# Optimization experiments

Hardware: AMD Instinct MI355X
Metric: run time of the kernel (lower is better)

Reference implementation:

```python
import jax, jax.numpy as jnp
import numpy as np

# physics constants (match init_kwargs)
DT = 1.0 / 60.0
G_ACC = 9.81
RHO = 1.225
CD = 0.47
NU = 0.001
B, N, GRID = 512, 64, 16


def _norm(x):
    return jnp.linalg.norm(x, axis=-1, keepdims=True)


def _deriv(pos, vel, rot, omega, mass, inertia, contacts, fluid_v,
           Fext, tau, log_A, log_k, log_b, conv_w):
    g_vec = jnp.array([0.0, 0.0, -G_ACC], dtype=pos.dtype)
    Fg = mass[..., None] * g_vec                                  # [B,N,3]
    A = jax.nn.softplus(log_A).reshape(1, -1, 1)
    vm = jnp.maximum(_norm(vel), 1e-6)
    Fd = -0.5 * RHO * CD * A * vm * vel                           # drag
    k = jax.nn.softplus(log_k)
    b = jax.nn.softplus(log_b)
    d_ij = pos[:, None, :, :] - pos[:, :, None, :]                # [B,N,N,3] = p_j - p_i
    dist = jnp.maximum(_norm(d_ij), 1e-6)
    n_hat = d_ij / dist
    pen = jax.nn.relu(1.0 - dist[..., 0])                         # penetration depth
    dvel = vel[:, None, :, :] - vel[:, :, None, :]                # v_j - v_i
    Fc = (k * pen[..., None] * n_hat + b * dvel * contacts[..., None]).sum(axis=2)
    dv = (Fext + Fg + Fd + Fc) / mass[..., None]
    Io = inertia * omega
    domega = (tau - jnp.cross(omega, Io)) / jnp.maximum(inertia, 1e-6)
    w, x, y, z = rot[..., 0], rot[..., 1], rot[..., 2], rot[..., 3]
    ox, oy, oz = omega[..., 0], omega[..., 1], omega[..., 2]
    drot = 0.5 * jnp.stack([
        -x * ox - y * oy - z * oz,
        w * ox + y * oz - z * oy,
        w * oy - x * oz + z * ox,
        w * oz + x * oy - y * ox], axis=-1)
    P_in = (Fext * vel).sum((-1, -2))
    P_dis = -(Fd * vel).sum((-1, -2))
    dE = P_in - P_dis
    Bsz = fluid_v.shape[0]
    u = fluid_v.reshape(Bsz, GRID, GRID, GRID, 3).transpose(0, 4, 1, 2, 3)  # NCDHW
    dfluid = NU * jax.lax.conv_general_dilated(
        u, conv_w, window_strides=(1, 1, 1), padding=[(1, 1)] * 3,
        feature_group_count=3,
        dimension_numbers=('NCDHW', 'OIDHW', 'NCDHW'))
    dfluid = dfluid.transpose(0, 2, 3, 4, 1).reshape(Bsz, GRID ** 3, 3)
    return vel, dv, drot, domega, dE, dfluid


def _quat_normalize(q):
    return q / jnp.maximum(_norm(q), 1e-12)


def _apply(pos, vel, rot, omega, fluid_v, dt, dp, dv, dr, dw, dfluid):
    npos = pos + dt * dp
    nvel = vel + dt * dv
    nrot = _quat_normalize(rot + dt * dr)
    nomega = omega + dt * dw
    new_u = fluid_v + dt * dfluid
    nfluid = new_u - new_u.mean(axis=1, keepdims=True)
    return npos, nvel, nrot, nomega, nfluid


def _forward(pos, vel, rot, omega, mass, inertia, contacts, energy, fluid_v,
             Fext, tau, log_A, log_k, log_b, conv_w):
    dt = DT
    params = (mass, inertia, contacts)

    def deriv(p, v, r, o, fv):
        return _deriv(p, v, r, o, mass, inertia, contacts, fv,
                      Fext, tau, log_A, log_k, log_b, conv_w)

    k1 = deriv(pos, vel, rot, omega, fluid_v)
    s2 = _apply(pos, vel, rot, omega, fluid_v, dt / 2, k1[0], k1[1], k1[2], k1[3], k1[5])
    k2 = deriv(*s2)
    s3 = _apply(pos, vel, rot, omega, fluid_v, dt / 2, k2[0], k2[1], k2[2], k2[3], k2[5])
    k3 = deriv(*s3)
    s4 = _apply(pos, vel, rot, omega, fluid_v, dt, k3[0], k3[1], k3[2], k3[3], k3[5])
    k4 = deriv(*s4)

    def rk4c(y, a, b_, c, d):
        return y + dt / 6 * (a + 2 * b_ + 2 * c + d)

    npos = rk4c(pos, k1[0], k2[0], k3[0], k4[0])
    nvel = rk4c(vel, k1[1], k2[1], k3[1], k4[1])
    nrot = _quat_normalize(rk4c(rot, k1[2], k2[2], k3[2], k4[2]))
    nomega = rk4c(omega, k1[3], k2[3], k3[3], k4[3])
    nenergy = rk4c(energy, k1[4], k2[4], k3[4], k4[4])
    nforces = Fext + mass[..., None] * k1[1]
    raw_fluid = rk4c(fluid_v, k1[5], k2[5], k3[5], k4[5])
    nfluid = raw_fluid - raw_fluid.mean(axis=1, keepdims=True)
    Bsz = pos.shape[0]
    # flatten new state: [pos, vel, rot, omega, forces, energy, fluid_v]
    return jnp.concatenate([
        npos.reshape(Bsz, -1), nvel.reshape(Bsz, -1), nrot.reshape(Bsz, -1),
        nomega.reshape(Bsz, -1), nforces.reshape(Bsz, -1),
        nenergy[:, None], nfluid.reshape(Bsz, -1)], axis=-1)


def setup_inputs() -> dict:
    key = jax.random.key(0)
    ks = jax.random.split(key, 12)
    rot = jax.random.normal(ks[2], (B, N, 4), dtype=jnp.float32)
    rot = rot / jnp.maximum(jnp.linalg.norm(rot, axis=-1, keepdims=True), 1e-12)
    return {
        'pos': 2.0 * jax.random.normal(ks[0], (B, N, 3), dtype=jnp.float32),
        'vel': jax.random.normal(ks[1], (B, N, 3), dtype=jnp.float32),
        'rot': rot,
        'omega': jax.random.normal(ks[3], (B, N, 3), dtype=jnp.float32),
        'mass': 0.5 + jax.random.uniform(ks[4], (B, N), dtype=jnp.float32),
        'inertia': 0.05 + 0.1 * jax.random.uniform(ks[5], (B, N, 3), dtype=jnp.float32),
        'contacts': jax.random.uniform(ks[6], (B, N, N), dtype=jnp.float32),
        'energy': jnp.zeros((B,), dtype=jnp.float32),
        'fluid_v': jax.random.normal(ks[7], (B, GRID ** 3, 3), dtype=jnp.float32),
        'Fext': jax.random.normal(ks[8], (B, N, 3), dtype=jnp.float32),
        'tau': jax.random.normal(ks[9], (B, N, 3), dtype=jnp.float32),
        'log_A': jnp.zeros((N,), dtype=jnp.float32),
        'log_k': jnp.full((1,), np.log(1000.0), dtype=jnp.float32),
        'log_b': jnp.full((1,), np.log(10.0), dtype=jnp.float32),
        'conv_w': 0.1 * jax.random.normal(ks[10], (3, 1, 3, 3, 3), dtype=jnp.float32),
    }


def reference(pos, vel, rot, omega, mass, inertia, contacts, energy, fluid_v,
              Fext, tau, log_A, log_k, log_b, conv_w):
    return _forward(pos, vel, rot, omega, mass, inertia, contacts, energy,
                    fluid_v, Fext, tau, log_A, log_k, log_b, conv_w)
```

## Files before the change

kernel.cpp:

```cpp
#include <hip/hip_runtime.h>

#define DT (1.0f/60.0f)
#define G_ACC 9.81f
#define RHO 1.225f
#define CD_ 0.47f
#define NU 0.001f

__device__ __forceinline__ float softplus_f(float x) {
    return log1pf(expf(-fabsf(x))) + fmaxf(x, 0.0f);
}

#define RL(v, l) __int_as_float(__builtin_amdgcn_readlane(__float_as_int(v), (l)))

__device__ __forceinline__ float dpp_xm(float v) {
    return __int_as_float(__builtin_amdgcn_update_dpp(0, __float_as_int(v), 0x111, 0xf, 0xf, true));
}
__device__ __forceinline__ float dpp_xp(float v) {
    return __int_as_float(__builtin_amdgcn_update_dpp(0, __float_as_int(v), 0x101, 0xf, 0xf, true));
}

__global__ __launch_bounds__(256) void fused_kernel(
    const float* __restrict__ pos, const float* __restrict__ vel,
    const float* __restrict__ rot, const float* __restrict__ omega,
    const float* __restrict__ mass, const float* __restrict__ inertia,
    const float* __restrict__ contacts, const float* __restrict__ energy,
    const float* __restrict__ fluid, const float* __restrict__ Fext,
    const float* __restrict__ tau, const float* __restrict__ log_A,
    const float* __restrict__ log_k, const float* __restrict__ log_b,
    const float* __restrict__ conv_w, float* __restrict__ out)
{
    __shared__ float smem[4384];
    const int t = threadIdx.x;

    if (blockIdx.x < 1536) {
        const int b  = blockIdx.x & 511;
        const int ch = blockIdx.x >> 9;
        const int x  = t & 15, y = t >> 4, wv = t >> 6;
        float* u   = smem;
        float* wch = smem + 4352;
        float* red = smem + 4380;
        if (t < 27) wch[t] = conv_w[ch*27 + t];

        const int lb = t*17;
        const float* fb = fluid + (size_t)b*12288 + 3*t + ch;
        float base[16], acc[16];
        #pragma unroll
        for (int z = 0; z < 16; ++z) {
            float v = fb[z*768];
            base[z] = v; acc[z] = 0.f; u[lb + z] = v;
        }
        __syncthreads();

        const float mm = (y > 0)  ? 1.f : 0.f;
        const float pm = (y < 15) ? 1.f : 0.f;
        const float xm = (x > 0)  ? 1.f : 0.f;
        const float xp = (x < 15) ? 1.f : 0.f;
        const int   cm = (y > 0)  ? lb - 272 : lb;
        const int   cp = (y < 15) ? lb + 272 : lb;

        float Sdz[3];
        #pragma unroll
        for (int dz = 0; dz < 3; ++dz) {
            float a0 = wch[dz*9+0]*xm + wch[dz*9+1] + wch[dz*9+2]*xp;
            float a1 = wch[dz*9+3]*xm + wch[dz*9+4] + wch[dz*9+5]*xp;
            float a2 = wch[dz*9+6]*xm + wch[dz*9+7] + wch[dz*9+8]*xp;
            Sdz[dz] = mm*a0 + a1 + pm*a2;
        }
        const float SzLo  = Sdz[1] + Sdz[2];
        const float SzMid = Sdz[0] + Sdz[1] + Sdz[2];
        const float SzHi  = Sdz[0] + Sdz[1];
        const float* W = wch + 0;

        const float wgt[4] = {1.f, 2.f, 2.f, 1.f};
        const float hs[3]  = {DT*0.5f, DT*0.5f, DT};
        float mean = 0.f;

        #define ACC3(c, wi) { \
            float w0_ = W[wi], w1_ = W[9+(wi)], w2_ = W[18+(wi)]; \
            _Pragma("unroll") for (int z = 0; z < 16; ++z) o[z] += w1_ * (c)[z]; \
            _Pragma("unroll") for (int z = 1; z < 16; ++z) o[z] += w0_ * (c)[z-1]; \
            _Pragma("unroll") for (int z = 0; z < 15; ++z) o[z] += w2_ * (c)[z+1]; }

        for (int s = 0; s < 4; ++s) {
            float o[16];
            #pragma unroll
            for (int z = 0; z < 16; ++z) o[z] = 0.f;

            {
                float c0[16], cl[16], cr[16];
                #pragma unroll
                for (int z = 0; z < 16; ++z) c0[z] = u[lb + z];
                #pragma unroll
                for (int z = 0; z < 16; ++z) { cl[z] = dpp_xm(c0[z]); cr[z] = dpp_xp(c0[z]); }
                ACC3(c0, 4); ACC3(cl, 3); ACC3(cr, 5);
            }
            {
                float c0[16], cl[16], cr[16];
                #pragma unroll
                for (int z = 0; z < 16; ++z) c0[z] = u[cm + z] * mm;
                #pragma unroll
                for (int z = 0; z < 16; ++z) { cl[z] = dpp_xm(c0[z]); cr[z] = dpp_xp(c0[z]); }
                ACC3(c0, 1); ACC3(cl, 0); ACC3(cr, 2);
            }
            {
                float c0[16], cl[16], cr[16];
                #pragma unroll
                for (int z = 0; z < 16; ++z) c0[z] = u[cp + z] * pm;
                #pragma unroll
                for (int z = 0; z < 16; ++z) { cl[z] = dpp_xm(c0[z]); cr[z] = dpp_xp(c0[z]); }
                ACC3(c0, 7); ACC3(cl, 6); ACC3(cr, 8);
            }

            float w = wgt[s];
            if (s < 3) {
                float h = hs[s], ps = 0.f, wn[16];
                #pragma unroll
                for (int z = 0; z < 16; ++z) {
                    float Sz = (z == 0) ? SzLo : ((z == 15) ? SzHi : SzMid);
                    float k = NU * (o[z] - mean * Sz);
                    acc[z] += w * k;
                    wn[z] = base[z] + h * k;
                    ps += wn[z];
                }
                #pragma unroll
                for (int off = 32; off > 0; off >>= 1) ps += __shfl_xor(ps, off, 64);
                __syncthreads();
                #pragma unroll
                for (int z = 0; z < 16; ++z) u[lb + z] = wn[z];
                if ((t & 63) == 0) red[wv] = ps;
                __syncthreads();
                mean = (red[0] + red[1] + red[2] + red[3]) * (1.0f/4096.0f);
            } else {
                #pragma unroll
                for (int z = 0; z < 16; ++z) {
                    float Sz = (z == 0) ? SzLo : ((z == 15) ? SzHi : SzMid);
                    acc[z] += w * NU * (o[z] - mean * Sz);
                }
            }
        }
        #undef ACC3

        float raw[16], ps = 0.f;
        #pragma unroll
        for (int z = 0; z < 16; ++z) { raw[z] = base[z] + (DT/6.0f)*acc[z]; ps += raw[z]; }
        #pragma unroll
        for (int off = 32; off > 0; off >>= 1) ps += __shfl_xor(ps, off, 64);
        __syncthreads();
        if ((t & 63) == 0) red[wv] = ps;
        __syncthreads();
        float mn = (red[0] + red[1] + red[2] + red[3]) * (1.0f/4096.0f);

        float* ob = out + (size_t)b*13313 + 1025 + 3*t + ch;
        #pragma unroll
        for (int z = 0; z < 16; ++z) ob[z*768] = raw[z] - mn;
        return;
    }

    const int b = blockIdx.x - 1536;
    const int q = t >> 6;
    const int i = t & 63;
    #define SF(buf, qq, idx) smem[(buf)*768 + (qq)*192 + (idx)]

    const float* cbase = contacts + (size_t)b*4096 + (size_t)i*64 + q*16;
    float4 cA = ((const float4*)cbase)[0];
    float4 cB = ((const float4*)cbase)[1];
    float4 cC = ((const float4*)cbase)[2];
    float4 cD = ((const float4*)cbase)[3];
    float cj[16] = {cA.x,cA.y,cA.z,cA.w, cB.x,cB.y,cB.z,cB.w,
                    cC.x,cC.y,cC.z,cC.w, cD.x,cD.y,cD.z,cD.w};

    const size_t p3 = ((size_t)b*64 + i)*3;
    const size_t p4 = ((size_t)b*64 + i)*4;
    float bpx=pos[p3],   bpy=pos[p3+1],   bpz=pos[p3+2];
    float bvx=vel[p3],   bvy=vel[p3+1],   bvz=vel[p3+2];
    float brw=rot[p4],   brx=rot[p4+1],   bry=rot[p4+2],  brz=rot[p4+3];
    float box=omega[p3], boy=omega[p3+1], boz=omega[p3+2];
    float m  = mass[(size_t)b*64+i];
    float Ix=inertia[p3], Iy=inertia[p3+1], Iz=inertia[p3+2];
    float Fex=Fext[p3],   Fey=Fext[p3+1],   Fez=Fext[p3+2];
    float tx=tau[p3],     ty=tau[p3+1],     tz=tau[p3+2];
    float Ai = softplus_f(log_A[i]);
    float kc = softplus_f(log_k[0]);
    float bc = softplus_f(log_b[0]);
    float dragc = -0.5f * RHO * CD_ * Ai;
    float invm  = 1.0f / m;
    float iIx = 1.0f/fmaxf(Ix,1e-6f), iIy = 1.0f/fmaxf(Iy,1e-6f), iIz = 1.0f/fmaxf(Iz,1e-6f);

    float cpx=bpx, cpy=bpy, cpz=bpz;
    float cvx=bvx, cvy=bvy, cvz=bvz;
    float crw=brw, crx=brx, cry=bry, crz=brz;
    float cox=box, coy=boy, coz=boz;

    float apx=0,apy=0,apz=0, avx=0,avy=0,avz=0;
    float arw=0,arx=0,ary=0,arz=0, awx=0,awy=0,awz=0;
    float eacc=0.f;
    float k1vx=0,k1vy=0,k1vz=0;

    const float wgt[4] = {1.f, 2.f, 2.f, 1.f};
    const float hs[4]  = {DT*0.5f, DT*0.5f, DT, 0.f};
    const int j0 = q << 4;

    for (int s = 0; s < 4; ++s) {
        float Fcx=0.f, Fcy=0.f, Fcz=0.f;
        #pragma unroll
        for (int jj = 0; jj < 16; ++jj) {
            const int j = j0 + jj;
            float pjx = RL(cpx, j), pjy = RL(cpy, j), pjz = RL(cpz, j);
            float vjx = RL(cvx, j), vjy = RL(cvy, j), vjz = RL(cvz, j);
            float dx = pjx - cpx, dy = pjy - cpy, dz = pjz - cpz;
            float d2 = dx*dx + dy*dy + dz*dz;
            float dist = fmaxf(sqrtf(d2), 1e-6f);
            float pen  = fmaxf(1.0f - dist, 0.0f);
            float coef = kc * pen * __builtin_amdgcn_rcpf(dist);
            float cbj  = bc * cj[jj];
            Fcx += coef*dx + cbj*(vjx - cvx);
            Fcy += coef*dy + cbj*(vjy - cvy);
            Fcz += coef*dz + cbj*(vjz - cvz);
        }
        const int buf = s & 1;
        SF(buf, q, i*3+0) = Fcx;
        SF(buf, q, i*3+1) = Fcy;
        SF(buf, q, i*3+2) = Fcz;
        __syncthreads();
        Fcx = SF(buf,0,i*3+0) + SF(buf,1,i*3+0) + SF(buf,2,i*3+0) + SF(buf,3,i*3+0);
        Fcy = SF(buf,0,i*3+1) + SF(buf,1,i*3+1) + SF(buf,2,i*3+1) + SF(buf,3,i*3+1);
        Fcz = SF(buf,0,i*3+2) + SF(buf,1,i*3+2) + SF(buf,2,i*3+2) + SF(buf,3,i*3+2);

        float vm = fmaxf(sqrtf(cvx*cvx+cvy*cvy+cvz*cvz), 1e-6f);
        float dc = dragc * vm;
        float Fdx = dc*cvx, Fdy = dc*cvy, Fdz = dc*cvz;

        float dvx = (Fex + Fdx + Fcx) * invm;
        float dvy = (Fey + Fdy + Fcy) * invm;
        float dvz = (Fez - m*G_ACC + Fdz + Fcz) * invm;

        float dqw = 0.5f*(-crx*cox - cry*coy - crz*coz);
        float dqx = 0.5f*( crw*cox + cry*coz - crz*coy);
        float dqy = 0.5f*( crw*coy - crx*coz + crz*cox);
        float dqz = 0.5f*( crw*coz + crx*coy - cry*cox);

        float Iox = Ix*cox, Ioy = Iy*coy, Ioz = Iz*coz;
        float cxv = coy*Ioz - coz*Ioy;
        float cyv = coz*Iox - cox*Ioz;
        float czv = cox*Ioy - coy*Iox;
        float dwx = (tx - cxv) * iIx;
        float dwy = (ty - cyv) * iIy;
        float dwz = (tz - czv) * iIz;

        float ei = (Fex+Fdx)*cvx + (Fey+Fdy)*cvy + (Fez+Fdz)*cvz;
        #pragma unroll
        for (int off = 32; off > 0; off >>= 1) ei += __shfl_xor(ei, off, 64);

        float w = wgt[s];
        eacc += w * ei;
        if (s == 0) { k1vx=dvx; k1vy=dvy; k1vz=dvz; }
        apx += w*cvx; apy += w*cvy; apz += w*cvz;
        avx += w*dvx; avy += w*dvy; avz += w*dvz;
        arw += w*dqw; arx += w*dqx; ary += w*dqy; arz += w*dqz;
        awx += w*dwx; awy += w*dwy; awz += w*dwz;

        if (s < 3) {
            float h = hs[s];
            float npx = bpx + h*cvx, npy = bpy + h*cvy, npz = bpz + h*cvz;
            cvx = bvx + h*dvx; cvy = bvy + h*dvy; cvz = bvz + h*dvz;
            cpx = npx; cpy = npy; cpz = npz;
            float qw = brw + h*dqw, qx = brx + h*dqx, qy = bry + h*dqy, qz = brz + h*dqz;
            float iqn = 1.0f / fmaxf(sqrtf(qw*qw+qx*qx+qy*qy+qz*qz), 1e-12f);
            crw = qw*iqn; crx = qx*iqn; cry = qy*iqn; crz = qz*iqn;
            cox = box + h*dwx; coy = boy + h*dwy; coz = boz + h*dwz;
        }
    }

    if (q == 0) {
        const float s6 = DT / 6.0f;
        float* ob = out + (size_t)b * 13313;
        ob[      i*3+0] = bpx + s6*apx;  ob[      i*3+1] = bpy + s6*apy;  ob[      i*3+2] = bpz + s6*apz;
        ob[192 + i*3+0] = bvx + s6*avx;  ob[192 + i*3+1] = bvy + s6*avy;  ob[192 + i*3+2] = bvz + s6*avz;
        {
            float qw=brw+s6*arw, qx=brx+s6*arx, qy=bry+s6*ary, qz=brz+s6*arz;
            float iq = 1.0f / fmaxf(sqrtf(qw*qw+qx*qx+qy*qy+qz*qz), 1e-12f);
            ob[384 + i*4+0]=qw*iq; ob[384 + i*4+1]=qx*iq; ob[384 + i*4+2]=qy*iq; ob[384 + i*4+3]=qz*iq;
        }
        ob[640 + i*3+0] = box + s6*awx;  ob[640 + i*3+1] = boy + s6*awy;  ob[640 + i*3+2] = boz + s6*awz;
        ob[832 + i*3+0] = Fex + m*k1vx;  ob[832 + i*3+1] = Fey + m*k1vy;  ob[832 + i*3+2] = Fez + m*k1vz;
        if (i == 0) ob[1024] = energy[b] + s6*eacc;
    }
    #undef SF
}

extern "C" void kernel_launch(void* const* d_in, const int* in_sizes, int n_in,
                              void* d_out, int out_size, void* d_ws, size_t ws_size,
                              hipStream_t stream) {
    const float* pos      = (const float*)d_in[0];
    const float* vel      = (const float*)d_in[1];
    const float* rot      = (const float*)d_in[2];
    const float* omega    = (const float*)d_in[3];
    const float* mass     = (const float*)d_in[4];
    const float* inertia  = (const float*)d_in[5];
    const float* contacts = (const float*)d_in[6];
    const float* energy   = (const float*)d_in[7];
    const float* fluid_v  = (const float*)d_in[8];
    const float* Fext     = (const float*)d_in[9];
    const float* tau      = (const float*)d_in[10];
    const float* log_A    = (const float*)d_in[11];
    const float* log_k    = (const float*)d_in[12];
    const float* log_b    = (const float*)d_in[13];
    const float* conv_w   = (const float*)d_in[14];
    float* out = (float*)d_out;

    fused_kernel<<<dim3(2048), dim3(256), 0, stream>>>(
        pos, vel, rot, omega, mass, inertia, contacts, energy, fluid_v,
        Fext, tau, log_A, log_k, log_b, conv_w, out);
}
```

Baseline: 159.0 us.

## Process all three fluid channels in one block per batch

Each fluid block now loops over the three velocity channels sequentially instead of launching one block per channel, cutting the grid from 2048 to 1024 blocks. Output stores are interleaved across channels, so each thread writes three contiguous floats per z rather than strided single floats. The cost is less parallelism, longer serial work per block, and more live registers (raw0, raw1, rloc), which may lower occupancy.

```diff
diff --git a/kernel.cpp b/kernel.cpp
--- a/kernel.cpp
+++ b/kernel.cpp
@@ -32,24 +32,13 @@
     __shared__ float smem[4384];
     const int t = threadIdx.x;
 
-    if (blockIdx.x < 1536) {
-        const int b  = blockIdx.x & 511;
-        const int ch = blockIdx.x >> 9;
+    if (blockIdx.x < 512) {
+        const int b  = blockIdx.x;
         const int x  = t & 15, y = t >> 4, wv = t >> 6;
         float* u   = smem;
         float* wch = smem + 4352;
         float* red = smem + 4380;
-        if (t < 27) wch[t] = conv_w[ch*27 + t];
-
         const int lb = t*17;
-        const float* fb = fluid + (size_t)b*12288 + 3*t + ch;
-        float base[16], acc[16];
-        #pragma unroll
-        for (int z = 0; z < 16; ++z) {
-            float v = fb[z*768];
-            base[z] = v; acc[z] = 0.f; u[lb + z] = v;
-        }
-        __syncthreads();
 
         const float mm = (y > 0)  ? 1.f : 0.f;
         const float pm = (y < 15) ? 1.f : 0.f;
@@ -58,22 +47,11 @@
         const int   cm = (y > 0)  ? lb - 272 : lb;
         const int   cp = (y < 15) ? lb + 272 : lb;
 
-        float Sdz[3];
-        #pragma unroll
-        for (int dz = 0; dz < 3; ++dz) {
-            float a0 = wch[dz*9+0]*xm + wch[dz*9+1] + wch[dz*9+2]*xp;
-            float a1 = wch[dz*9+3]*xm + wch[dz*9+4] + wch[dz*9+5]*xp;
-            float a2 = wch[dz*9+6]*xm + wch[dz*9+7] + wch[dz*9+8]*xp;
-            Sdz[dz] = mm*a0 + a1 + pm*a2;
-        }
-        const float SzLo  = Sdz[1] + Sdz[2];
-        const float SzMid = Sdz[0] + Sdz[1] + Sdz[2];
-        const float SzHi  = Sdz[0] + Sdz[1];
-        const float* W = wch + 0;
-
         const float wgt[4] = {1.f, 2.f, 2.f, 1.f};
         const float hs[3]  = {DT*0.5f, DT*0.5f, DT};
-        float mean = 0.f;
+
+        float raw0[16], raw1[16], rloc[16];
+        float mn0 = 0.f, mn1 = 0.f, mn2 = 0.f;
 
         #define ACC3(c, wi) { \
             float w0_ = W[wi], w1_ = W[9+(wi)], w2_ = W[18+(wi)]; \
@@ -81,82 +59,124 @@
             _Pragma("unroll") for (int z = 1; z < 16; ++z) o[z] += w0_ * (c)[z-1]; \
             _Pragma("unroll") for (int z = 0; z < 15; ++z) o[z] += w2_ * (c)[z+1]; }
 
-        for (int s = 0; s < 4; ++s) {
-            float o[16];
+        for (int ch = 0; ch < 3; ++ch) {
+            if (t < 27) wch[t] = conv_w[ch*27 + t];
+            const float* fb = fluid + (size_t)b*12288 + 3*t + ch;
+            float base[16], acc[16];
             #pragma unroll
-            for (int z = 0; z < 16; ++z) o[z] = 0.f;
-
-            {
-                float c0[16], cl[16], cr[16];
+            for (int z = 0; z < 16; ++z) {
+                float v = fb[z*768];
+                base[z] = v; acc[z] = 0.f; u[lb + z] = v;
+            }
+            __syncthreads();
+
+            float Sdz[3];
+            #pragma unroll
+            for (int dz = 0; dz < 3; ++dz) {
+                float a0 = wch[dz*9+0]*xm + wch[dz*9+1] + wch[dz*9+2]*xp;
+                float a1 = wch[dz*9+3]*xm + wch[dz*9+4] + wch[dz*9+5]*xp;
+                float a2 = wch[dz*9+6]*xm + wch[dz*9+7] + wch[dz*9+8]*xp;
+                Sdz[dz] = mm*a0 + a1 + pm*a2;
+            }
+            const float SzLo  = Sdz[1] + Sdz[2];
+            const float SzMid = Sdz[0] + Sdz[1] + Sdz[2];
+            const float SzHi  = Sdz[0] + Sdz[1];
+            const float* W = wch;
+            float mean = 0.f;
+
+            for (int s = 0; s < 4; ++s) {
+                float o[16];
                 #pragma unroll
-                for (int z = 0; z < 16; ++z) c0[z] = u[lb + z];
-                #pragma unroll
-                for (int z = 0; z < 16; ++z) { cl[z] = dpp_xm(c0[z]); cr[z] = dpp_xp(c0[z]); }
-                ACC3(c0, 4); ACC3(cl, 3); ACC3(cr, 5);
-            }
-            {
-                float c0[16], cl[16], cr[16];
-                #pragma unroll
-                for (int z = 0; z < 16; ++z) c0[z] = u[cm + z] * mm;
-                #pragma unroll
-                for (int z = 0; z < 16; ++z) { cl[z] = dpp_xm(c0[z]); cr[z] = dpp_xp(c0[z]); }
-                ACC3(c0, 1); ACC3(cl, 0); ACC3(cr, 2);
-            }
-            {
-                float c0[16], cl[16], cr[16];
-                #pragma unroll
-                for (int z = 0; z < 16; ++z) c0[z] = u[cp + z] * pm;
-                #pragma unroll
-                for (int z = 0; z < 16; ++z) { cl[z] = dpp_xm(c0[z]); cr[z] = dpp_xp(c0[z]); }
-                ACC3(c0, 7); ACC3(cl, 6); ACC3(cr, 8);
-            }
-
-            float w = wgt[s];
-            if (s < 3) {
-                float h = hs[s], ps = 0.f, wn[16];
-                #pragma unroll
-                for (int z = 0; z < 16; ++z) {
-                    float Sz = (z == 0) ? SzLo : ((z == 15) ? SzHi : SzMid);
-                    float k = NU * (o[z] - mean * Sz);
-                    acc[z] += w * k;
-                    wn[z] = base[z] + h * k;
-                    ps += wn[z];
+                for (int z = 0; z < 16; ++z) o[z] = 0.f;
+
+                {
+                    float c0[16], cl[16], cr[16];
+                    #pragma unroll
+                    for (int z = 0; z < 16; ++z) c0[z] = u[lb + z];
+                    #pragma unroll
+                    for (int z = 0; z < 16; ++z) { cl[z] = dpp_xm(c0[z]); cr[z] = dpp_xp(c0[z]); }
+                    ACC3(c0, 4); ACC3(cl, 3); ACC3(cr, 5);
                 }
-                #pragma unroll
-                for (int off = 32; off > 0; off >>= 1) ps += __shfl_xor(ps, off, 64);
-                __syncthreads();
-                #pragma unroll
-                for (int z = 0; z < 16; ++z) u[lb + z] = wn[z];
-                if ((t & 63) == 0) red[wv] = ps;
-                __syncthreads();
-                mean = (red[0] + red[1] + red[2] + red[3]) * (1.0f/4096.0f);
-            } else {
-                #pragma unroll
-                for (int z = 0; z < 16; ++z) {
-                    float Sz = (z == 0) ? SzLo : ((z == 15) ? SzHi : SzMid);
-                    acc[z] += w * NU * (o[z] - mean * Sz);
+                {
+                    float c0[16], cl[16], cr[16];
+                    #pragma unroll
+                    for (int z = 0; z < 16; ++z) c0[z] = u[cm + z] * mm;
+                    #pragma unroll
+                    for (int z = 0; z < 16; ++z) { cl[z] = dpp_xm(c0[z]); cr[z] = dpp_xp(c0[z]); }
+                    ACC3(c0, 1); ACC3(cl, 0); ACC3(cr, 2);
+                }
+                {
+                    float c0[16], cl[16], cr[16];
+                    #pragma unroll
+                    for (int z = 0; z < 16; ++z) c0[z] = u[cp + z] * pm;
+                    #pragma unroll
+                    for (int z = 0; z < 16; ++z) { cl[z] = dpp_xm(c0[z]); cr[z] = dpp_xp(c0[z]); }
+                    ACC3(c0, 7); ACC3(cl, 6); ACC3(cr, 8);
+                }
+
+                float w = wgt[s];
+                if (s < 3) {
+                    float h = hs[s], ps = 0.f, wn[16];
+                    #pragma unroll
+                    for (int z = 0; z < 16; ++z) {
+                        float Sz = (z == 0) ? SzLo : ((z == 15) ? SzHi : SzMid);
+                        float k = NU * (o[z] - mean * Sz);
+                        acc[z] += w * k;
+                        wn[z] = base[z] + h * k;
+                        ps += wn[z];
+                    }
+                    #pragma unroll
+                    for (int off = 32; off > 0; off >>= 1) ps += __shfl_xor(ps, off, 64);
+                    __syncthreads();
+                    #pragma unroll
+                    for (int z = 0; z < 16; ++z) u[lb + z] = wn[z];
+                    if ((t & 63) == 0) red[wv] = ps;
+                    __syncthreads();
+                    mean = (red[0] + red[1] + red[2] + red[3]) * (1.0f/4096.0f);
+                } else {
+                    #pragma unroll
+                    for (int z = 0; z < 16; ++z) {
+                        float Sz = (z == 0) ? SzLo : ((z == 15) ? SzHi : SzMid);
+                        acc[z] += w * NU * (o[z] - mean * Sz);
+                    }
                 }
             }
+
+            float ps = 0.f;
+            #pragma unroll
+            for (int z = 0; z < 16; ++z) { rloc[z] = base[z] + (DT/6.0f)*acc[z]; ps += rloc[z]; }
+            #pragma unroll
+            for (int off = 32; off > 0; off >>= 1) ps += __shfl_xor(ps, off, 64);
+            __syncthreads();
+            if ((t & 63) == 0) red[wv] = ps;
+            __syncthreads();
+            float mn = (red[0] + red[1] + red[2] + red[3]) * (1.0f/4096.0f);
+
+            if (ch == 0) {
+                #pragma unroll
+                for (int z = 0; z < 16; ++z) raw0[z] = rloc[z];
+                mn0 = mn;
+            } else if (ch == 1) {
+                #pragma unroll
+                for (int z = 0; z < 16; ++z) raw1[z] = rloc[z];
+                mn1 = mn;
+            } else {
+                mn2 = mn;
+            }
         }
         #undef ACC3
 
-        float raw[16], ps = 0.f;
+        float* ob = out + (size_t)b*13313 + 1025 + 3*t;
         #pragma unroll
-        for (int z = 0; z < 16; ++z) { raw[z] = base[z] + (DT/6.0f)*acc[z]; ps += raw[z]; }
-        #pragma unroll
-        for (int off = 32; off > 0; off >>= 1) ps += __shfl_xor(ps, off, 64);
-        __syncthreads();
-        if ((t & 63) == 0) red[wv] = ps;
-        __syncthreads();
-        float mn = (red[0] + red[1] + red[2] + red[3]) * (1.0f/4096.0f);
-
-        float* ob = out + (size_t)b*13313 + 1025 + 3*t + ch;
-        #pragma unroll
-        for (int z = 0; z < 16; ++z) ob[z*768] = raw[z] - mn;
+        for (int z = 0; z < 16; ++z) {
+            ob[z*768 + 0] = raw0[z] - mn0;
+            ob[z*768 + 1] = raw1[z] - mn1;
+            ob[z*768 + 2] = rloc[z] - mn2;
+        }
         return;
     }
 
-    const int b = blockIdx.x - 1536;
+    const int b = blockIdx.x - 512;
     const int q = t >> 6;
     const int i = t & 63;
     #define SF(buf, qq, idx) smem[(buf)*768 + (qq)*192 + (idx)]
@@ -308,7 +328,7 @@
     const float* conv_w   = (const float*)d_in[14];
     float* out = (float*)d_out;
 
-    fused_kernel<<<dim3(2048), dim3(256), 0, stream>>>(
+    fused_kernel<<<dim3(1024), dim3(256), 0, stream>>>(
         pos, vel, rot, omega, mass, inertia, contacts, energy, fluid_v,
         Fext, tau, log_A, log_k, log_b, conv_w, out);
 }
```

Result: slower. 176.9 us (+11.2%).
